# Kernel tuning notes

Measured on AMD Instinct MI355X. Metric: run time of the kernel, lower is better.

The kernel has to match this reference:

```python
import jax, jax.numpy as jnp
import numpy as np

EPS = 1e-6
K_HOPS = 2  # SGConv K


def setup_inputs() -> dict:
    key = jax.random.key(0)
    k1, k2, k3, k4 = jax.random.split(key, 4)
    B, Kk, C, T = 32, 8, 64, 250
    E, H = 4096, 128
    x = jax.random.normal(k1, (B, Kk, C, T), dtype=jnp.float32)
    edge_index = jax.random.randint(k2, (2, E), 0, C, dtype=jnp.int64)
    edge_weights = jax.random.uniform(k3, (E,), dtype=jnp.float32)
    W = jax.random.normal(k4, (H, Kk * T), dtype=jnp.float32) * 0.02
    b = jnp.zeros((H,), dtype=jnp.float32)
    return {"x": x, "edge_index": edge_index, "edge_weights": edge_weights, "W": W, "b": b}


def reference(x, edge_index, edge_weights, W, b):
    B, Kk, C, T = x.shape
    N = C  # nodes
    x = x.reshape(B, N, Kk * T)  # (B, N, F)

    # clamp non-positive edge weights to epsilon (mirrors in-place .data clamp)
    w = jnp.where(edge_weights <= 0, EPS, edge_weights)

    # gcn_norm with self loops (fill value 1.0)
    src, dst = edge_index[0], edge_index[1]
    loop = jnp.arange(N, dtype=edge_index.dtype)
    src = jnp.concatenate([src, loop])
    dst = jnp.concatenate([dst, loop])
    w = jnp.concatenate([w, jnp.ones((N,), w.dtype)])
    deg = jnp.zeros((N,), w.dtype).at[dst].add(w)
    dinv = jnp.where(deg > 0, deg ** -0.5, jnp.zeros_like(deg))
    norm = dinv[src] * w * dinv[dst]  # (E+N,)

    # K hops of gather -> weight -> scatter-add aggregation
    for _ in range(K_HOPS):
        msg = x[:, src, :] * norm[None, :, None]        # (B, E+N, F)
        x = jnp.zeros_like(x).at[:, dst, :].add(msg)    # (B, N, F)

    # final linear: y = x @ W^T + b
    return jnp.einsum('bnf,hf->bnh', x, W) + b
```

## Files before the change

kernel.cpp:

```cpp
#include <hip/hip_runtime.h>
#include <hip/hip_bf16.h>

#define EPSW 1e-6f

typedef __attribute__((ext_vector_type(4))) float floatx4;
typedef __attribute__((ext_vector_type(8))) short shortx8;

__device__ __forceinline__ unsigned short f2bf(float f) {
    unsigned int u = __float_as_uint(f);
    u = (u + 0x7fffu + ((u >> 16) & 1u)) >> 16;
    return (unsigned short)u;
}

__global__ __launch_bounds__(256) void prep(const float* __restrict__ x,
                                            const float* __restrict__ W,
                                            const int* __restrict__ ei,
                                            const float* __restrict__ ew,
                                            unsigned short* __restrict__ xt,
                                            unsigned short* __restrict__ wt,
                                            float* __restrict__ Mt) {
    __shared__ __align__(16) unsigned char smem[64 * 264 * 2];
    const int bid = blockIdx.x;
    const int t   = threadIdx.x;

    if (bid < 256) {
        unsigned short(*tile)[264] = (unsigned short(*)[264])smem;
        const int rb   = (bid >> 3) * 64;
        const int kgb  = (bid & 7) * 32;
        const int kbas = kgb * 8;
#pragma unroll
        for (int i = 0; i < 16; ++i) {
            const int idx = i * 256 + t;
            const int r   = idx >> 6;
            const int kc  = (idx & 63) * 4;
            const int k   = kbas + kc;
            floatx4 v = (floatx4){0.f, 0.f, 0.f, 0.f};
            if (k < 2000)
                v = *(const floatx4*)(x + (size_t)(rb + r) * 2000 + k);
            tile[r][kc + 0] = f2bf(v.x);
            tile[r][kc + 1] = f2bf(v.y);
            tile[r][kc + 2] = f2bf(v.z);
            tile[r][kc + 3] = f2bf(v.w);
        }
        __syncthreads();
#pragma unroll
        for (int i = 0; i < 8; ++i) {
            const int kg_l = i * 4 + (t >> 6);
            const int r    = t & 63;
            const shortx8 g = *(const shortx8*)&tile[r][kg_l * 8];
            *(shortx8*)(xt + ((size_t)(kgb + kg_l) * 2048 + rb + r) * 8) = g;
        }
    } else if (bid < 272) {
#pragma unroll
        for (int i = 0; i < 8; ++i) {
            const int G  = (bid - 256) * 2048 + i * 256 + t;
            const int kg = G >> 7;
            const int h  = G & 127;
            const int k  = kg * 8;
            floatx4 v0 = (floatx4){0.f, 0.f, 0.f, 0.f};
            floatx4 v1 = (floatx4){0.f, 0.f, 0.f, 0.f};
            if (k < 2000) {
                v0 = *(const floatx4*)(W + (size_t)h * 2000 + k);
                v1 = *(const floatx4*)(W + (size_t)h * 2000 + k + 4);
            }
            unsigned short* p = wt + ((size_t)kg * 128 + h) * 8;
            p[0] = f2bf(v0.x); p[1] = f2bf(v0.y); p[2] = f2bf(v0.z); p[3] = f2bf(v0.w);
            p[4] = f2bf(v1.x); p[5] = f2bf(v1.y); p[6] = f2bf(v1.z); p[7] = f2bf(v1.w);
        }
    } else {
        float* A    = (float*)smem;
        float* deg  = (float*)(smem + 16384);
        float* dinv = deg + 64;
        if (t < 64) deg[t] = 1.0f;
        for (int i = t; i < 4096; i += 256) A[i] = 0.0f;
        __syncthreads();
        const int* src = ei;
        const int* dst = ei + 4096;
        for (int e = t; e < 4096; e += 256) {
            float w = ew[e];
            w = (w <= 0.0f) ? EPSW : w;
            atomicAdd(&deg[dst[e]], w);
        }
        __syncthreads();
        if (t < 64) dinv[t] = 1.0f / sqrtf(deg[t]);
        __syncthreads();
        for (int e = t; e < 4096; e += 256) {
            float w = ew[e];
            w = (w <= 0.0f) ? EPSW : w;
            const int s = src[e], d = dst[e];
            atomicAdd(&A[d * 64 + s], dinv[s] * w * dinv[d]);
        }
        if (t < 64) atomicAdd(&A[t * 64 + t], dinv[t] * dinv[t]);
        __syncthreads();
#pragma unroll
        for (int i = 0; i < 16; ++i) {
            const int idx = i * 256 + t;
            const int n = idx >> 6, c = idx & 63;
            float s = 0.0f;
#pragma unroll 8
            for (int k = 0; k < 64; ++k) s += A[n * 64 + k] * A[k * 64 + c];
            Mt[c * 64 + n] = s;
        }
    }
}

__global__ __launch_bounds__(512) void gemm_apply(
        const unsigned short* __restrict__ xt,
        const unsigned short* __restrict__ wt,
        const float* __restrict__ Mt,
        const float* __restrict__ bias,
        float* __restrict__ y) {
    __shared__ float Ms[4096];
    __shared__ float zs[64][17];
    const int t    = threadIdx.x;
    const int wave = t >> 6, lane = t & 63;
    const int m = lane & 15, q = lane >> 4;
    const int ht = blockIdx.x;
    const int b  = blockIdx.y;
    const int rt = wave & 3, kh = wave >> 2;

    {
        const floatx4* Mg4 = (const floatx4*)Mt;
        floatx4* Ms4 = (floatx4*)Ms;
        Ms4[t]       = Mg4[t];
        Ms4[t + 512] = Mg4[t + 512];
    }

    const shortx8* Ag = (const shortx8*)xt;
    const shortx8* Bg = (const shortx8*)wt;
    int ga = (kh * 128 + q) * 2048 + b * 64 + rt * 16 + m;
    int gb = (kh * 128 + q) * 128 + ht * 16 + m;

    floatx4 acc0 = (floatx4){0.f, 0.f, 0.f, 0.f};
    floatx4 acc1 = (floatx4){0.f, 0.f, 0.f, 0.f};
#pragma unroll 4
    for (int kt = 0; kt < 32; kt += 2) {
        const shortx8 a0 = Ag[ga];
        const shortx8 b0 = Bg[gb];
        const shortx8 a1 = Ag[ga + 8192];
        const shortx8 b1 = Bg[gb + 512];
        acc0 = __builtin_amdgcn_mfma_f32_16x16x32_bf16(a0, b0, acc0, 0, 0, 0);
        acc1 = __builtin_amdgcn_mfma_f32_16x16x32_bf16(a1, b1, acc1, 0, 0, 0);
        ga += 16384; gb += 1024;
    }
    acc0 += acc1;

    __syncthreads();
    if (kh == 0) {
#pragma unroll
        for (int v = 0; v < 4; ++v) zs[rt * 16 + q * 4 + v][m] = acc0[v];
    }
    __syncthreads();
    if (kh == 1) {
#pragma unroll
        for (int v = 0; v < 4; ++v) zs[rt * 16 + q * 4 + v][m] += acc0[v];
    }
    __syncthreads();

    {
        const int n0 = t >> 4;
        const int h  = t & 15;
        const float bv = bias[ht * 16 + h];
        float s0 = bv, s1 = bv;
#pragma unroll
        for (int mm = 0; mm < 64; ++mm) {
            const float zv = zs[mm][h];
            s0 += Ms[mm * 64 + n0]      * zv;
            s1 += Ms[mm * 64 + n0 + 32] * zv;
        }
        float* yp = y + (size_t)b * 8192 + ht * 16 + h;
        yp[(size_t)n0 * 128]        = s0;
        yp[(size_t)(n0 + 32) * 128] = s1;
    }
}

extern "C" void kernel_launch(void* const* d_in, const int* in_sizes, int n_in,
                              void* d_out, int out_size, void* d_ws, size_t ws_size,
                              hipStream_t stream) {
    const float* x    = (const float*)d_in[0];
    const int*   ei   = (const int*)d_in[1];
    const float* ew   = (const float*)d_in[2];
    const float* W    = (const float*)d_in[3];
    const float* bias = (const float*)d_in[4];
    float* y = (float*)d_out;

    float* Mt = (float*)d_ws;
    unsigned short* xt = (unsigned short*)(Mt + 4096);
    unsigned short* wt = xt + 4194304;

    prep<<<273, 256, 0, stream>>>(x, W, ei, ew, xt, wt, Mt);
    gemm_apply<<<dim3(8, 32), 512, 0, stream>>>(xt, wt, Mt, bias, y);
}
```

Before: 102.5 us.

## Stage GEMM operands through LDS with double-buffered direct global-to-LDS loads

Operand tiles for the GEMM are now fetched with global_load_lds DMA into double-buffered shared memory, so the next chunk can load while the current one is consumed by MFMA. The prep kernel moves to 512-thread blocks, and the grid is flattened so blocks sharing a W tile sit next to each other. The loop now waits on all outstanding memory and adds two barriers per chunk, which can serialise the pipeline and cancel the intended overlap.

After: 100.7 us. Within noise of the previous version (-1.7%).

```diff
diff --git a/kernel.cpp b/kernel.cpp
--- a/kernel.cpp
+++ b/kernel.cpp
@@ -12,7 +12,13 @@
     return (unsigned short)u;
 }
 
-__global__ __launch_bounds__(256) void prep(const float* __restrict__ x,
+__device__ __forceinline__ void gl_lds16(const void* g, void* l) {
+    __builtin_amdgcn_global_load_lds(
+        (const __attribute__((address_space(1))) unsigned int*)g,
+        (__attribute__((address_space(3))) unsigned int*)l, 16, 0, 0);
+}
+
+__global__ __launch_bounds__(512) void prep(const float* __restrict__ x,
                                             const float* __restrict__ W,
                                             const int* __restrict__ ei,
                                             const float* __restrict__ ew,
@@ -29,8 +35,8 @@
         const int kgb  = (bid & 7) * 32;
         const int kbas = kgb * 8;
 #pragma unroll
-        for (int i = 0; i < 16; ++i) {
-            const int idx = i * 256 + t;
+        for (int i = 0; i < 8; ++i) {
+            const int idx = i * 512 + t;
             const int r   = idx >> 6;
             const int kc  = (idx & 63) * 4;
             const int k   = kbas + kc;
@@ -44,16 +50,16 @@
         }
         __syncthreads();
 #pragma unroll
-        for (int i = 0; i < 8; ++i) {
-            const int kg_l = i * 4 + (t >> 6);
+        for (int i = 0; i < 4; ++i) {
+            const int kg_l = i * 8 + (t >> 6);
             const int r    = t & 63;
             const shortx8 g = *(const shortx8*)&tile[r][kg_l * 8];
             *(shortx8*)(xt + ((size_t)(kgb + kg_l) * 2048 + rb + r) * 8) = g;
         }
     } else if (bid < 272) {
 #pragma unroll
-        for (int i = 0; i < 8; ++i) {
-            const int G  = (bid - 256) * 2048 + i * 256 + t;
+        for (int i = 0; i < 4; ++i) {
+            const int G  = (bid - 256) * 2048 + i * 512 + t;
             const int kg = G >> 7;
             const int h  = G & 127;
             const int k  = kg * 8;
@@ -72,29 +78,33 @@
         float* deg  = (float*)(smem + 16384);
         float* dinv = deg + 64;
         if (t < 64) deg[t] = 1.0f;
-        for (int i = t; i < 4096; i += 256) A[i] = 0.0f;
-        __syncthreads();
-        const int* src = ei;
-        const int* dst = ei + 4096;
-        for (int e = t; e < 4096; e += 256) {
+        for (int i = t; i < 4096; i += 512) A[i] = 0.0f;
+        __syncthreads();
+        const int* srcp = ei;
+        const int* dstp = ei + 4096;
+#pragma unroll
+        for (int i = 0; i < 8; ++i) {
+            const int e = i * 512 + t;
             float w = ew[e];
             w = (w <= 0.0f) ? EPSW : w;
-            atomicAdd(&deg[dst[e]], w);
+            atomicAdd(&deg[dstp[e]], w);
         }
         __syncthreads();
         if (t < 64) dinv[t] = 1.0f / sqrtf(deg[t]);
         __syncthreads();
-        for (int e = t; e < 4096; e += 256) {
+#pragma unroll
+        for (int i = 0; i < 8; ++i) {
+            const int e = i * 512 + t;
             float w = ew[e];
             w = (w <= 0.0f) ? EPSW : w;
-            const int s = src[e], d = dst[e];
+            const int s = srcp[e], d = dstp[e];
             atomicAdd(&A[d * 64 + s], dinv[s] * w * dinv[d]);
         }
         if (t < 64) atomicAdd(&A[t * 64 + t], dinv[t] * dinv[t]);
         __syncthreads();
 #pragma unroll
-        for (int i = 0; i < 16; ++i) {
-            const int idx = i * 256 + t;
+        for (int i = 0; i < 8; ++i) {
+            const int idx = i * 512 + t;
             const int n = idx >> 6, c = idx & 63;
             float s = 0.0f;
 #pragma unroll 8
@@ -104,20 +114,24 @@
     }
 }
 
-__global__ __launch_bounds__(512) void gemm_apply(
+__global__ __launch_bounds__(512) void gemm_dma_apply(
         const unsigned short* __restrict__ xt,
         const unsigned short* __restrict__ wt,
         const float* __restrict__ Mt,
         const float* __restrict__ bias,
         float* __restrict__ y) {
+    __shared__ __align__(16) unsigned char xbuf[2][8192];
+    __shared__ __align__(16) unsigned char wbuf[2][2048];
     __shared__ float Ms[4096];
     __shared__ float zs[64][17];
     const int t    = threadIdx.x;
     const int wave = t >> 6, lane = t & 63;
     const int m = lane & 15, q = lane >> 4;
-    const int ht = blockIdx.x;
-    const int b  = blockIdx.y;
+    const int bid = blockIdx.x;
+    const int b   = bid & 31;
+    const int ht  = bid >> 5;
     const int rt = wave & 3, kh = wave >> 2;
+    const int rbase = b * 64;
 
     {
         const floatx4* Mg4 = (const floatx4*)Mt;
@@ -126,26 +140,38 @@
         Ms4[t + 512] = Mg4[t + 512];
     }
 
-    const shortx8* Ag = (const shortx8*)xt;
-    const shortx8* Bg = (const shortx8*)wt;
-    int ga = (kh * 128 + q) * 2048 + b * 64 + rt * 16 + m;
-    int gb = (kh * 128 + q) * 128 + ht * 16 + m;
+#define ISSUE_CHUNK(c)                                                        \
+    {                                                                         \
+        const int ckg = (c) * 8;                                              \
+        unsigned char* xb = xbuf[(c) & 1];                                    \
+        unsigned char* wb = wbuf[(c) & 1];                                    \
+        gl_lds16(xt + ((size_t)(ckg + wave) * 2048 + rbase + lane) * 8,       \
+                 xb + wave * 1024);                                           \
+        if (wave < 2)                                                         \
+            gl_lds16(wt + ((size_t)(ckg + wave * 4 + (lane >> 4)) * 128 +     \
+                           ht * 16 + (lane & 15)) * 8,                        \
+                     wb + wave * 1024);                                       \
+    }
 
     floatx4 acc0 = (floatx4){0.f, 0.f, 0.f, 0.f};
     floatx4 acc1 = (floatx4){0.f, 0.f, 0.f, 0.f};
-#pragma unroll 4
-    for (int kt = 0; kt < 32; kt += 2) {
-        const shortx8 a0 = Ag[ga];
-        const shortx8 b0 = Bg[gb];
-        const shortx8 a1 = Ag[ga + 8192];
-        const shortx8 b1 = Bg[gb + 512];
-        acc0 = __builtin_amdgcn_mfma_f32_16x16x32_bf16(a0, b0, acc0, 0, 0, 0);
-        acc1 = __builtin_amdgcn_mfma_f32_16x16x32_bf16(a1, b1, acc1, 0, 0, 0);
-        ga += 16384; gb += 1024;
+
+    ISSUE_CHUNK(0);
+    for (int c = 0; c < 32; ++c) {
+        __builtin_amdgcn_s_waitcnt(0);
+        __syncthreads();
+        if (c < 31) ISSUE_CHUNK(c + 1);
+        const unsigned char* xb = xbuf[c & 1];
+        const unsigned char* wb = wbuf[c & 1];
+        const int kgl = kh * 4 + q;
+        const shortx8 af = *(const shortx8*)(xb + kgl * 1024 + (rt * 16 + m) * 16);
+        const shortx8 bf = *(const shortx8*)(wb + kgl * 256 + m * 16);
+        if (c & 1) acc1 = __builtin_amdgcn_mfma_f32_16x16x32_bf16(af, bf, acc1, 0, 0, 0);
+        else       acc0 = __builtin_amdgcn_mfma_f32_16x16x32_bf16(af, bf, acc0, 0, 0, 0);
+        __syncthreads();
     }
     acc0 += acc1;
 
-    __syncthreads();
     if (kh == 0) {
 #pragma unroll
         for (int v = 0; v < 4; ++v) zs[rt * 16 + q * 4 + v][m] = acc0[v];
@@ -156,7 +182,6 @@
         for (int v = 0; v < 4; ++v) zs[rt * 16 + q * 4 + v][m] += acc0[v];
     }
     __syncthreads();
-
     {
         const int n0 = t >> 4;
         const int h  = t & 15;
@@ -188,6 +213,6 @@
     unsigned short* xt = (unsigned short*)(Mt + 4096);
     unsigned short* wt = xt + 4194304;
 
-    prep<<<273, 256, 0, stream>>>(x, W, ei, ew, xt, wt, Mt);
-    gemm_apply<<<dim3(8, 32), 512, 0, stream>>>(xt, wt, Mt, bias, y);
-}
+    prep<<<273, 512, 0, stream>>>(x, W, ei, ew, xt, wt, Mt);
+    gemm_dma_apply<<<256, 512, 0, stream>>>(xt, wt, Mt, bias, y);
+}
```
